# Performance work log

Hardware: AMD Instinct MI355X
Metric: run time of the kernel (lower is better)

Reference implementation:

```python
import jax, jax.numpy as jnp
import numpy as np

B, L, H = 32, 1024, 1024


def setup_inputs() -> dict:
    key = jax.random.key(0)
    ks = jax.random.split(key, 6)
    s = 1.0 / np.sqrt(H)
    return {
        "query": jax.random.normal(ks[0], (B, L, H), dtype=jnp.float32),
        "key": jax.random.normal(ks[1], (B, L, H), dtype=jnp.float32),
        "value": jax.random.normal(ks[2], (B, L, H), dtype=jnp.float32),
        "W": jax.random.normal(ks[3], (H, H), dtype=jnp.float32) * s,
        "mlp_w": jax.random.normal(ks[4], (1, 2 * H), dtype=jnp.float32) * s,
        "mlp_b": jnp.zeros((1,), dtype=jnp.float32),
    }


def reference(query, key, value, W, mlp_w, mlp_b):
    # Shared projection W (Linear, no bias): x @ W.T
    q = jnp.einsum("blh,oh->blo", query, W)
    k = jnp.einsum("blh,oh->blo", key, W)
    v = jnp.einsum("blh,oh->blo", value, W)
    # sim_mlp(cat([q,k],-1)) == q @ w1.T + k @ w2.T + b  (avoids materializing concat)
    w1, w2 = mlp_w[:, :H], mlp_w[:, H:]  # each [1, H]
    logits = jax.nn.relu(
        jnp.einsum("blh,oh->blo", q, w1) + jnp.einsum("blh,oh->blo", k, w2) + mlp_b
    )  # [B, L, 1]
    score = jax.nn.softmax(logits, axis=-2)  # softmax over L
    result = jnp.sum(score * v, axis=-2)  # [B, H]
    return result, score
```

## Files before the change

### kernel.cpp

```cpp
#include <hip/hip_runtime.h>

#define HDIM 1024
#define BDIM 32
#define LDIM 1024


__global__ __launch_bounds__(256) void k_u12(const float* __restrict__ W,
                                             const float* __restrict__ mlp_w,
                                             float* __restrict__ u1,
                                             float* __restrict__ u2) {
    int h  = blockIdx.x * 256 + threadIdx.x;
    int o0 = blockIdx.y * 128;
    float s1 = 0.f, s2 = 0.f;
    #pragma unroll 8
    for (int o = o0; o < o0 + 128; ++o) {
        float w = W[o * HDIM + h];
        s1 += w * mlp_w[o];
        s2 += w * mlp_w[HDIM + o];
    }
    atomicAdd(&u1[h], s1);
    atomicAdd(&u2[h], s2);
}

__global__ __launch_bounds__(256) void k_logits(const float4* __restrict__ q,
                                                const float4* __restrict__ k,
                                                const float* __restrict__ u1,
                                                const float* __restrict__ u2,
                                                const float* __restrict__ mlp_b,
                                                float* __restrict__ logits) {
    __shared__ float4 su1[256];
    __shared__ float4 su2[256];
    int t = threadIdx.x;
    su1[t] = ((const float4*)u1)[t];
    su2[t] = ((const float4*)u2)[t];
    __syncthreads();
    int wave = t >> 6, lane = t & 63;
    long long row = (long long)blockIdx.x * 4 + wave;
    const float4* qr = q + row * 256;
    const float4* kr = k + row * 256;
    float acc = 0.f;
    #pragma unroll
    for (int i = 0; i < 4; ++i) {
        int idx = lane + 64 * i;
        float4 a  = qr[idx];
        float4 b1 = su1[idx];
        acc += a.x * b1.x + a.y * b1.y + a.z * b1.z + a.w * b1.w;
        float4 c  = kr[idx];
        float4 b2 = su2[idx];
        acc += c.x * b2.x + c.y * b2.y + c.z * b2.z + c.w * b2.w;
    }
    #pragma unroll
    for (int off = 32; off > 0; off >>= 1)
        acc += __shfl_down(acc, off, 64);
    if (lane == 0) {
        float v = acc + mlp_b[0];
        logits[row] = v > 0.f ? v : 0.f;
    }
}

__global__ __launch_bounds__(256) void k_softmax(const float* __restrict__ logits,
                                                 float* __restrict__ score) {
    __shared__ float sm[4];
    __shared__ float ss[4];
    int b = blockIdx.x;
    int t = threadIdx.x;
    int wave = t >> 6, lane = t & 63;
    float4 v = ((const float4*)(logits + b * LDIM))[t];
    float m = fmaxf(fmaxf(v.x, v.y), fmaxf(v.z, v.w));
    #pragma unroll
    for (int off = 32; off > 0; off >>= 1)
        m = fmaxf(m, __shfl_down(m, off, 64));
    if (lane == 0) sm[wave] = m;
    __syncthreads();
    float M = fmaxf(fmaxf(sm[0], sm[1]), fmaxf(sm[2], sm[3]));
    float4 e;
    e.x = __expf(v.x - M); e.y = __expf(v.y - M);
    e.z = __expf(v.z - M); e.w = __expf(v.w - M);
    float s = e.x + e.y + e.z + e.w;
    #pragma unroll
    for (int off = 32; off > 0; off >>= 1)
        s += __shfl_down(s, off, 64);
    if (lane == 0) ss[wave] = s;
    __syncthreads();
    float inv = 1.f / (ss[0] + ss[1] + ss[2] + ss[3]);
    float4 o;
    o.x = e.x * inv; o.y = e.y * inv; o.z = e.z * inv; o.w = e.w * inv;
    ((float4*)(score + b * LDIM))[t] = o;
}

__global__ __launch_bounds__(256) void k_vbar(const float4* __restrict__ value,
                                              const float* __restrict__ score,
                                              float* __restrict__ vbar) {
    int b  = blockIdx.x >> 4;
    int lc = blockIdx.x & 15;
    int t  = threadIdx.x;
    const float4* vrow = value + ((long long)b * LDIM + lc * 64) * 256 + t;
    const float*  sc   = score + b * LDIM + lc * 64;
    float4 acc = make_float4(0.f, 0.f, 0.f, 0.f);
    #pragma unroll 8
    for (int l = 0; l < 64; ++l) {
        float s  = sc[l];
        float4 v = vrow[(long long)l * 256];
        acc.x += s * v.x; acc.y += s * v.y; acc.z += s * v.z; acc.w += s * v.w;
    }
    float* dst = vbar + b * HDIM + t * 4;
    atomicAdd(dst + 0, acc.x);
    atomicAdd(dst + 1, acc.y);
    atomicAdd(dst + 2, acc.z);
    atomicAdd(dst + 3, acc.w);
}

__global__ __launch_bounds__(256) void k_result(const float* __restrict__ W,
                                                const float* __restrict__ vbar,
                                                float* __restrict__ result) {
    __shared__ float4 sv[256];
    int b  = blockIdx.x >> 3;
    int oc = blockIdx.x & 7;
    int t  = threadIdx.x;
    sv[t] = ((const float4*)(vbar + b * HDIM))[t];
    __syncthreads();
    int wave = t >> 6, lane = t & 63;
    for (int o = oc * 128 + wave; o < oc * 128 + 128; o += 4) {
        const float4* wr = (const float4*)(W + o * HDIM);
        float acc = 0.f;
        #pragma unroll
        for (int i = 0; i < 4; ++i) {
            int idx = lane + 64 * i;
            float4 w = wr[idx];
            float4 v = sv[idx];
            acc += w.x * v.x + w.y * v.y + w.z * v.z + w.w * v.w;
        }
        #pragma unroll
        for (int off = 32; off > 0; off >>= 1)
            acc += __shfl_down(acc, off, 64);
        if (lane == 0) result[b * HDIM + o] = acc;
    }
}

extern "C" void kernel_launch(void* const* d_in, const int* in_sizes, int n_in,
                              void* d_out, int out_size, void* d_ws, size_t ws_size,
                              hipStream_t stream) {
    const float* query = (const float*)d_in[0];
    const float* key   = (const float*)d_in[1];
    const float* value = (const float*)d_in[2];
    const float* W     = (const float*)d_in[3];
    const float* mlp_w = (const float*)d_in[4];
    const float* mlp_b = (const float*)d_in[5];

    float* out    = (float*)d_out;
    float* result = out;
    float* score  = out + BDIM * LDIM;

    float* u1     = (float*)d_ws;
    float* u2     = u1 + HDIM;
    float* vbar   = u2 + HDIM;
    float* logits = vbar + BDIM * HDIM;

    hipMemsetAsync(d_ws, 0, (size_t)(2 * HDIM + BDIM * HDIM) * sizeof(float), stream);

    k_u12<<<dim3(4, 8), 256, 0, stream>>>(W, mlp_w, u1, u2);
    k_logits<<<(BDIM * LDIM) / 4, 256, 0, stream>>>((const float4*)query, (const float4*)key,
                                                    u1, u2, mlp_b, logits);
    k_softmax<<<BDIM, 256, 0, stream>>>(logits, score);
    k_vbar<<<BDIM * 16, 256, 0, stream>>>((const float4*)value, score, vbar);
    k_result<<<BDIM * 8, 256, 0, stream>>>(W, vbar, result);
}
```

Measured before the change: 399.5 us.

## Restructure all four GEMV kernels for register reuse and vectorized loads

k_u12 now uses float4 loads of W over 64 blocks. k_logits keeps u1/u2 in registers and handles 4 rows per wave, which removes the shared-memory staging and barrier. k_vbar splits into two accumulators for more ILP. k_result loads each W row once into registers and loops over all batches, so W is read once instead of 32 times. The aim is fewer redundant loads and better memory-level parallelism in what is a bandwidth-bound pipeline. The cost is lower block counts and higher register pressure.

New measurement: 379.2 us. -5.1%, faster.

```diff
diff --git a/kernel.cpp b/kernel.cpp
--- a/kernel.cpp
+++ b/kernel.cpp
@@ -5,56 +5,65 @@
 #define LDIM 1024
 
 
-__global__ __launch_bounds__(256) void k_u12(const float* __restrict__ W,
+__global__ __launch_bounds__(256) void k_u12(const float4* __restrict__ W4,
                                              const float* __restrict__ mlp_w,
                                              float* __restrict__ u1,
                                              float* __restrict__ u2) {
-    int h  = blockIdx.x * 256 + threadIdx.x;
-    int o0 = blockIdx.y * 128;
-    float s1 = 0.f, s2 = 0.f;
-    #pragma unroll 8
-    for (int o = o0; o < o0 + 128; ++o) {
-        float w = W[o * HDIM + h];
-        s1 += w * mlp_w[o];
-        s2 += w * mlp_w[HDIM + o];
+    int t  = threadIdx.x;
+    int o0 = blockIdx.x * 16;
+    float4 s1 = make_float4(0.f, 0.f, 0.f, 0.f);
+    float4 s2 = make_float4(0.f, 0.f, 0.f, 0.f);
+    #pragma unroll 4
+    for (int o = o0; o < o0 + 16; ++o) {
+        float4 w = W4[o * 256 + t];
+        float c1 = mlp_w[o];
+        float c2 = mlp_w[HDIM + o];
+        s1.x += w.x * c1; s1.y += w.y * c1; s1.z += w.z * c1; s1.w += w.w * c1;
+        s2.x += w.x * c2; s2.y += w.y * c2; s2.z += w.z * c2; s2.w += w.w * c2;
     }
-    atomicAdd(&u1[h], s1);
-    atomicAdd(&u2[h], s2);
+    int h = t * 4;
+    atomicAdd(&u1[h + 0], s1.x); atomicAdd(&u1[h + 1], s1.y);
+    atomicAdd(&u1[h + 2], s1.z); atomicAdd(&u1[h + 3], s1.w);
+    atomicAdd(&u2[h + 0], s2.x); atomicAdd(&u2[h + 1], s2.y);
+    atomicAdd(&u2[h + 2], s2.z); atomicAdd(&u2[h + 3], s2.w);
 }
 
-__global__ __launch_bounds__(256) void k_logits(const float4* __restrict__ q,
-                                                const float4* __restrict__ k,
-                                                const float* __restrict__ u1,
-                                                const float* __restrict__ u2,
-                                                const float* __restrict__ mlp_b,
-                                                float* __restrict__ logits) {
-    __shared__ float4 su1[256];
-    __shared__ float4 su2[256];
+__global__ __launch_bounds__(256, 4) void k_logits(const float4* __restrict__ q,
+                                                   const float4* __restrict__ k,
+                                                   const float4* __restrict__ u1v,
+                                                   const float4* __restrict__ u2v,
+                                                   const float* __restrict__ mlp_b,
+                                                   float* __restrict__ logits) {
     int t = threadIdx.x;
-    su1[t] = ((const float4*)u1)[t];
-    su2[t] = ((const float4*)u2)[t];
-    __syncthreads();
-    int wave = t >> 6, lane = t & 63;
-    long long row = (long long)blockIdx.x * 4 + wave;
-    const float4* qr = q + row * 256;
-    const float4* kr = k + row * 256;
-    float acc = 0.f;
+    int lane = t & 63, wave = t >> 6;
+    float4 a1[4], a2[4];
     #pragma unroll
     for (int i = 0; i < 4; ++i) {
-        int idx = lane + 64 * i;
-        float4 a  = qr[idx];
-        float4 b1 = su1[idx];
-        acc += a.x * b1.x + a.y * b1.y + a.z * b1.z + a.w * b1.w;
-        float4 c  = kr[idx];
-        float4 b2 = su2[idx];
-        acc += c.x * b2.x + c.y * b2.y + c.z * b2.z + c.w * b2.w;
+        a1[i] = u1v[lane + 64 * i];
+        a2[i] = u2v[lane + 64 * i];
     }
-    #pragma unroll
-    for (int off = 32; off > 0; off >>= 1)
-        acc += __shfl_down(acc, off, 64);
-    if (lane == 0) {
-        float v = acc + mlp_b[0];
-        logits[row] = v > 0.f ? v : 0.f;
+    float bias = mlp_b[0];
+    long long wid = (long long)blockIdx.x * 4 + wave;
+    #pragma unroll 2
+    for (int r = 0; r < 4; ++r) {
+        long long row = wid * 4 + r;
+        const float4* qr = q + row * 256;
+        const float4* kr = k + row * 256;
+        float acc = 0.f;
+        #pragma unroll
+        for (int i = 0; i < 4; ++i) {
+            float4 x = qr[lane + 64 * i];
+            acc += x.x * a1[i].x + x.y * a1[i].y + x.z * a1[i].z + x.w * a1[i].w;
+            float4 y = kr[lane + 64 * i];
+            acc += y.x * a2[i].x + y.y * a2[i].y + y.z * a2[i].z + y.w * a2[i].w;
+        }
+        #pragma unroll
+        for (int off = 32; off > 0; off >>= 1)
+            acc += __shfl_down(acc, off, 64);
+        if (lane == 0) {
+            float v = acc + bias;
+            logits[row] = v > 0.f ? v : 0.f;
+        }
     }
 }
 
@@ -88,52 +97,60 @@
     ((float4*)(score + b * LDIM))[t] = o;
 }
 
-__global__ __launch_bounds__(256) void k_vbar(const float4* __restrict__ value,
-                                              const float* __restrict__ score,
-                                              float* __restrict__ vbar) {
+__global__ __launch_bounds__(256, 4) void k_vbar(const float4* __restrict__ value,
+                                                 const float* __restrict__ score,
+                                                 float* __restrict__ vbar) {
     int b  = blockIdx.x >> 4;
     int lc = blockIdx.x & 15;
     int t  = threadIdx.x;
     const float4* vrow = value + ((long long)b * LDIM + lc * 64) * 256 + t;
     const float*  sc   = score + b * LDIM + lc * 64;
-    float4 acc = make_float4(0.f, 0.f, 0.f, 0.f);
-    #pragma unroll 8
-    for (int l = 0; l < 64; ++l) {
-        float s  = sc[l];
-        float4 v = vrow[(long long)l * 256];
-        acc.x += s * v.x; acc.y += s * v.y; acc.z += s * v.z; acc.w += s * v.w;
+    float4 acc0 = make_float4(0.f, 0.f, 0.f, 0.f);
+    float4 acc1 = make_float4(0.f, 0.f, 0.f, 0.f);
+    #pragma unroll 4
+    for (int l = 0; l < 64; l += 2) {
+        float s0  = sc[l];
+        float4 v0 = vrow[(long long)l * 256];
+        acc0.x += s0 * v0.x; acc0.y += s0 * v0.y; acc0.z += s0 * v0.z; acc0.w += s0 * v0.w;
+        float s1  = sc[l + 1];
+        float4 v1 = vrow[(long long)(l + 1) * 256];
+        acc1.x += s1 * v1.x; acc1.y += s1 * v1.y; acc1.z += s1 * v1.z; acc1.w += s1 * v1.w;
     }
     float* dst = vbar + b * HDIM + t * 4;
-    atomicAdd(dst + 0, acc.x);
-    atomicAdd(dst + 1, acc.y);
-    atomicAdd(dst + 2, acc.z);
-    atomicAdd(dst + 3, acc.w);
+    atomicAdd(dst + 0, acc0.x + acc1.x);
+    atomicAdd(dst + 1, acc0.y + acc1.y);
+    atomicAdd(dst + 2, acc0.z + acc1.z);
+    atomicAdd(dst + 3, acc0.w + acc1.w);
 }
 
-__global__ __launch_bounds__(256) void k_result(const float* __restrict__ W,
-                                                const float* __restrict__ vbar,
-                                                float* __restrict__ result) {
-    __shared__ float4 sv[256];
-    int b  = blockIdx.x >> 3;
-    int oc = blockIdx.x & 7;
-    int t  = threadIdx.x;
-    sv[t] = ((const float4*)(vbar + b * HDIM))[t];
-    __syncthreads();
-    int wave = t >> 6, lane = t & 63;
-    for (int o = oc * 128 + wave; o < oc * 128 + 128; o += 4) {
-        const float4* wr = (const float4*)(W + o * HDIM);
-        float acc = 0.f;
+__global__ __launch_bounds__(256, 4) void k_result(const float4* __restrict__ W4,
+                                                   const float4* __restrict__ vbar4,
+                                                   float* __restrict__ result) {
+    int t = threadIdx.x;
+    int lane = t & 63, wave = t >> 6;
+    int o = blockIdx.x * 4 + wave;
+    float4 w[4];
+    #pragma unroll
+    for (int i = 0; i < 4; ++i)
+        w[i] = W4[o * 256 + lane + 64 * i];
+    for (int b = 0; b < BDIM; b += 2) {
+        float acc0 = 0.f, acc1 = 0.f;
         #pragma unroll
         for (int i = 0; i < 4; ++i) {
-            int idx = lane + 64 * i;
-            float4 w = wr[idx];
-            float4 v = sv[idx];
-            acc += w.x * v.x + w.y * v.y + w.z * v.z + w.w * v.w;
+            float4 v0 = vbar4[b * 256 + lane + 64 * i];
+            acc0 += v0.x * w[i].x + v0.y * w[i].y + v0.z * w[i].z + v0.w * w[i].w;
+            float4 v1 = vbar4[(b + 1) * 256 + lane + 64 * i];
+            acc1 += v1.x * w[i].x + v1.y * w[i].y + v1.z * w[i].z + v1.w * w[i].w;
         }
         #pragma unroll
-        for (int off = 32; off > 0; off >>= 1)
-            acc += __shfl_down(acc, off, 64);
-        if (lane == 0) result[b * HDIM + o] = acc;
+        for (int off = 32; off > 0; off >>= 1) {
+            acc0 += __shfl_down(acc0, off, 64);
+            acc1 += __shfl_down(acc1, off, 64);
+        }
+        if (lane == 0) {
+            result[b * HDIM + o]       = acc0;
+            result[(b + 1) * HDIM + o] = acc1;
+        }
     }
 }
 
@@ -158,10 +175,10 @@
 
     hipMemsetAsync(d_ws, 0, (size_t)(2 * HDIM + BDIM * HDIM) * sizeof(float), stream);
 
-    k_u12<<<dim3(4, 8), 256, 0, stream>>>(W, mlp_w, u1, u2);
-    k_logits<<<(BDIM * LDIM) / 4, 256, 0, stream>>>((const float4*)query, (const float4*)key,
-                                                    u1, u2, mlp_b, logits);
+    k_u12<<<64, 256, 0, stream>>>((const float4*)W, mlp_w, u1, u2);
+    k_logits<<<2048, 256, 0, stream>>>((const float4*)query, (const float4*)key,
+                                       (const float4*)u1, (const float4*)u2, mlp_b, logits);
     k_softmax<<<BDIM, 256, 0, stream>>>(logits, score);
     k_vbar<<<BDIM * 16, 256, 0, stream>>>((const float4*)value, score, vbar);
-    k_result<<<BDIM * 8, 256, 0, stream>>>(W, vbar, result);
+    k_result<<<256, 256, 0, stream>>>((const float4*)W, (const float4*)vbar, out);
 }
```
